# Kernel optimization log

Hardware: AMD Instinct MI355X
Metric: run time of the kernel (lower is better)

The kernel has to match this reference:

```python
import jax, jax.numpy as jnp
import numpy as np

N = 4096        # n_locations
D_MODEL = 512
H, D_K, D_V = 4, 128, 256


def setup_inputs() -> dict:
    key = jax.random.key(0)
    ks = jax.random.split(key, 7)
    s = 0.02
    return {
        "Q": jax.random.normal(ks[0], (N, D_MODEL), dtype=jnp.float32),
        "K": jax.random.normal(ks[1], (N, D_MODEL), dtype=jnp.float32),
        "V": jax.random.normal(ks[2], (N, D_MODEL), dtype=jnp.float32),
        "Wq": jax.random.normal(ks[3], (H, D_MODEL, D_K), dtype=jnp.float32) * s,
        "Wk": jax.random.normal(ks[4], (H, D_MODEL, D_K), dtype=jnp.float32) * s,
        "Wv": jax.random.normal(ks[5], (H, D_MODEL, D_V), dtype=jnp.float32) * s,
        "Wo": jax.random.normal(ks[6], (D_MODEL, H * D_V), dtype=jnp.float32) * s,
    }


def reference(Q, K, V, Wq, Wk, Wv, Wo):
    n = K.shape[0]
    # Batched per-head projections: [h, n, d_k] / [h, n, d_v]
    q = jnp.einsum('nd,hdk->hnk', Q, Wq)
    k = jnp.einsum('nd,hdk->hnk', K, Wk)
    v = jnp.einsum('nd,hdv->hnv', V, Wv)
    # NOTE: original scales by sqrt(n_locations) (K.size(0)), not sqrt(d_k)
    scores = jnp.einsum('hqk,hnk->hqn', q, k) / jnp.sqrt(jnp.asarray(n, q.dtype))
    weights = jax.nn.softmax(scores, axis=-1)          # [h, n, n]
    heads = jnp.einsum('hqn,hnv->hqv', weights, v)      # [h, n, d_v]
    # concat heads along feature dim: [n, h*d_v]
    x = jnp.transpose(heads, (1, 0, 2)).reshape(heads.shape[1], -1)
    return x @ Wo.T                                     # [n, d_model]
```

## Files before the change

### kernel.cpp

```cpp
#include <hip/hip_runtime.h>
#include <hip/hip_bf16.h>
#include <type_traits>

typedef __hip_bfloat16 bf16;
typedef __attribute__((ext_vector_type(8))) short bf16x8;
typedef __attribute__((ext_vector_type(4))) float f32x4;

#define N_LOC 4096

__device__ __forceinline__ bf16 to_bf16(float f) { return __float2bfloat16(f); }

__device__ __forceinline__ void dma16(const bf16* g, bf16* l) {
  __builtin_amdgcn_global_load_lds((const __attribute__((address_space(1))) unsigned int*)g,
                                   (__attribute__((address_space(3))) unsigned int*)l, 16, 0, 0);
}

__global__ __launch_bounds__(256) void prep(const float* __restrict__ Q, const float* __restrict__ K,
                                            const float* __restrict__ V, const float* __restrict__ Wo,
                                            bf16* __restrict__ Qb, bf16* __restrict__ Kb,
                                            bf16* __restrict__ Vb, bf16* __restrict__ Wob,
                                            const float* __restrict__ Wq, const float* __restrict__ Wk,
                                            const float* __restrict__ Wv,
                                            bf16* __restrict__ oq, bf16* __restrict__ ok,
                                            bf16* __restrict__ ov) {
  __shared__ float tile[64][65];
  if (blockIdx.x < 3328) {
    long i = ((long)blockIdx.x * 256 + threadIdx.x) * 8;
    const float* src;
    bf16* dst;
    long off;
    if (i < 2097152)      { src = Q;  dst = Qb;  off = i; }
    else if (i < 4194304) { src = K;  dst = Kb;  off = i - 2097152; }
    else if (i < 6291456) { src = V;  dst = Vb;  off = i - 4194304; }
    else                  { src = Wo; dst = Wob; off = i - 6291456; }
    float4 a = *(const float4*)&src[off];
    float4 b = *(const float4*)&src[off + 4];
    union { bf16 h[8]; bf16x8 v; } u;
    u.h[0] = to_bf16(a.x); u.h[1] = to_bf16(a.y); u.h[2] = to_bf16(a.z); u.h[3] = to_bf16(a.w);
    u.h[4] = to_bf16(b.x); u.h[5] = to_bf16(b.y); u.h[6] = to_bf16(b.z); u.h[7] = to_bf16(b.w);
    *(bf16x8*)&dst[off] = u.v;
  } else {
    int pid = blockIdx.x - 3328;
    int z = pid >> 7;
    int rem = pid & 127;
    int xx = rem & 7, y = rem >> 3;
    const float* W = (z == 0) ? Wq : (z == 1) ? Wk : Wv;
    bf16* out = (z == 0) ? oq : (z == 1) ? ok : ov;
    int DH = (z == 2) ? 256 : 128;
    int nt = DH >> 6;
    if (y >= 4 * nt) return;
    int h = y / nt, tt = y - h * nt;
    int d0 = xx * 64, t0 = tt * 64;
    for (int i = threadIdx.x; i < 4096; i += 256) {
      int r = i >> 6, c = i & 63;
      tile[r][c] = W[((size_t)h * 512 + d0 + r) * DH + t0 + c];
    }
    __syncthreads();
    for (int i = threadIdx.x; i < 4096; i += 256) {
      int t = i >> 6, d = i & 63;
      out[((size_t)(h * DH + t0 + t)) * 512 + d0 + d] = to_bf16(tile[d][t]);
    }
  }
}

template <int BN, int MODE, typename OutT>
__device__ __forceinline__ void gemm_body(const bf16* __restrict__ A, const bf16* __restrict__ Bt,
                                          OutT* __restrict__ C, int N, int K, int m0, int n0,
                                          bf16* sm) {
  constexpr int WN = BN / 2, JN = WN / 16, NB = BN / 32;
  int tid = threadIdx.x, lane = tid & 63, w = tid >> 6;
  int quad = lane >> 4, l16 = lane & 15;
  int wm = (w >> 1) * 64, wn = (w & 1) * WN;
  int srow = lane >> 3;
  int sG = (lane & 7) ^ srow;

  bf16* Asb[2] = { sm, sm + 8192 };
  bf16* Bsb[2] = { sm + 16384, sm + 16384 + BN * 64 };

  const bf16* ga[4];
  const bf16* gb[NB];
#pragma unroll
  for (int j = 0; j < 4; j++) ga[j] = A + (long)(m0 + (4 * j + w) * 8 + srow) * K + sG * 8;
#pragma unroll
  for (int j = 0; j < NB; j++) gb[j] = Bt + (long)(n0 + (4 * j + w) * 8 + srow) * K + sG * 8;

  auto stage = [&](int b) {
#pragma unroll
    for (int j = 0; j < 4; j++) { dma16(ga[j], &Asb[b][(4 * j + w) * 512]); ga[j] += 64; }
#pragma unroll
    for (int j = 0; j < NB; j++) { dma16(gb[j], &Bsb[b][(4 * j + w) * 512]); gb[j] += 64; }
  };

  f32x4 acc[4][JN] = {};
  stage(0);
  asm volatile("" ::: "memory");
  int cur = 0;
  const int NK = K >> 6;
  for (int s = 0; s < NK; ++s) {
    if (s + 1 < NK) {
      stage(cur ^ 1);
      if constexpr (NB == 4) asm volatile("s_waitcnt vmcnt(8)" ::: "memory");
      else                   asm volatile("s_waitcnt vmcnt(6)" ::: "memory");
    } else {
      asm volatile("s_waitcnt vmcnt(0)" ::: "memory");
    }
    __builtin_amdgcn_s_barrier();
    asm volatile("" ::: "memory");
    const bf16* Ac = Asb[cur];
    const bf16* Bc = Bsb[cur];
#pragma unroll
    for (int kk = 0; kk < 2; kk++) {
      bf16x8 af[4], bfr[JN];
#pragma unroll
      for (int i = 0; i < 4; i++) {
        int r = wm + i * 16 + l16;
        af[i] = *(const bf16x8*)&Ac[r * 64 + (((kk * 4 + quad) ^ r) & 7) * 8];
      }
#pragma unroll
      for (int j = 0; j < JN; j++) {
        int r = wn + j * 16 + l16;
        bfr[j] = *(const bf16x8*)&Bc[r * 64 + (((kk * 4 + quad) ^ r) & 7) * 8];
      }
#pragma unroll
      for (int i = 0; i < 4; i++)
#pragma unroll
        for (int j = 0; j < JN; j++)
          acc[i][j] = __builtin_amdgcn_mfma_f32_16x16x32_bf16(af[i], bfr[j], acc[i][j], 0, 0, 0);
    }
    asm volatile("" ::: "memory");
    __builtin_amdgcn_s_barrier();
    asm volatile("" ::: "memory");
    cur ^= 1;
  }

  if constexpr (MODE == 2) {
    bf16* tp = sm;
#pragma unroll
    for (int i = 0; i < 4; i++)
#pragma unroll
      for (int j = 0; j < JN; j++)
#pragma unroll
        for (int r = 0; r < 4; r++)
          tp[(wn + j * 16 + l16) * 136 + wm + i * 16 + quad * 4 + r] = to_bf16(acc[i][j][r]);
    __syncthreads();
#pragma unroll
    for (int it = 0; it < 8; ++it) {
      int idx = it * 256 + tid;
      int rown = idx >> 4, c8 = (idx & 15) * 8;
      *(bf16x8*)&C[(size_t)(n0 + rown) * 4096 + m0 + c8] = *(const bf16x8*)&tp[rown * 136 + c8];
    }
  } else {
#pragma unroll
    for (int i = 0; i < 4; i++)
#pragma unroll
      for (int j = 0; j < JN; j++)
#pragma unroll
        for (int r = 0; r < 4; r++) {
          long row = m0 + wm + i * 16 + quad * 4 + r;
          long col = n0 + wn + j * 16 + l16;
          if constexpr (MODE == 0)
            C[row * N + col] = to_bf16(acc[i][j][r]);
          else
            C[row * N + col] = acc[i][j][r];
        }
  }
}

__global__ __launch_bounds__(256) void proj_gemm(const bf16* __restrict__ QKVb,
                                                 const bf16* __restrict__ Wt,
                                                 bf16* __restrict__ qkout,
                                                 bf16* __restrict__ vTout) {
  __shared__ __align__(16) bf16 sm[4 * 128 * 64];
  int bid = blockIdx.x;
  if (bid < 256) {
    int z = bid >> 7;
    int t = bid & 127;
    int m0 = (t & 31) * 128, n0 = (t >> 5) * 128;
    gemm_body<128, 0, bf16>(QKVb + (size_t)z * 2097152, Wt + (size_t)z * 262144,
                            qkout + (size_t)z * 2097152, 512, 512, m0, n0, sm);
  } else {
    int t = bid - 256;
    int m0 = (t & 31) * 128, n0 = (t >> 5) * 128;
    gemm_body<128, 2, bf16>(QKVb + (size_t)2 * 2097152, Wt + (size_t)2 * 262144,
                            vTout, 1024, 512, m0, n0, sm);
  }
}

__global__ __launch_bounds__(256) void out_gemm(const bf16* __restrict__ xin,
                                                const bf16* __restrict__ Wob,
                                                float* __restrict__ outp) {
  __shared__ __align__(16) bf16 sm[2 * 128 * 64 + 2 * 64 * 64];
  gemm_body<64, 1, float>(xin, Wob, outp, 512, 1024, blockIdx.x * 128, blockIdx.y * 64, sm);
}

__global__ __launch_bounds__(256, 2) void attn(const bf16* __restrict__ qb,
                                               const bf16* __restrict__ kb,
                                               const bf16* __restrict__ vT,
                                               bf16* __restrict__ x) {
  __shared__ __align__(16) bf16 kt[2][64 * 128];
  __shared__ __align__(16) bf16 vt[2][128 * 64];
  __shared__ __align__(16) bf16 pt[4 * 16 * 72];

  const int bid = blockIdx.x;
  const int xcd = bid & 7;
  const int head = xcd & 3;
  const int dvh = xcd >> 2;
  const int q0 = (bid >> 3) * 64;
  const int tid = threadIdx.x;
  const int lane = tid & 63, w = tid >> 6;
  const int quad = lane >> 4, l16 = lane & 15;
  const int qw = q0 + w * 16;
  bf16* ptw = &pt[w * 16 * 72];

  bf16x8 qfB[4];
  {
    const bf16* qrow = &qb[(size_t)(qw + l16) * 512 + head * 128];
#pragma unroll
    for (int kk = 0; kk < 4; kk++) qfB[kk] = *(const bf16x8*)&qrow[kk * 32 + quad * 8];
  }

  f32x4 oacc[8] = {};
  float Lp = 0.0f;
  const float scale = 1.0f / 64.0f;

  const bf16* kpa[4];
  const bf16* vpa[4];
#pragma unroll
  for (int t2 = 0; t2 < 4; t2++) {
    int j = 4 * w + t2;
    {
      int r = 4 * j + (lane >> 4);
      int p = lane & 15;
      int G = (p & 8) | ((p ^ r) & 7);
      kpa[t2] = kb + (size_t)r * 512 + head * 128 + G * 8;
    }
    {
      int r = 8 * j + (lane >> 3);
      int p = lane & 7;
      int G = (p ^ r) & 7;
      vpa[t2] = vT + (size_t)(head * 256 + dvh * 128 + r) * 4096 + G * 8;
    }
  }
  auto STAGE = [&](int b) {
#pragma unroll
    for (int t2 = 0; t2 < 4; t2++) {
      dma16(kpa[t2], &kt[b][(4 * w + t2) * 512]); kpa[t2] += 64 * 512;
      dma16(vpa[t2], &vt[b][(4 * w + t2) * 512]); vpa[t2] += 64;
    }
  };

  STAGE(0);
  asm volatile("" ::: "memory");
  int cur = 0;

  for (int t = 0; t < 64; ++t) {
    asm volatile("s_waitcnt vmcnt(0)" ::: "memory");
    __builtin_amdgcn_s_barrier();
    asm volatile("" ::: "memory");
    if (t < 63) STAGE(cur ^ 1);

    const bf16* ktc = kt[cur];
    f32x4 sacc[4] = {};
#pragma unroll
    for (int kb4 = 0; kb4 < 4; kb4++) {
      int R = kb4 * 16 + l16;
#pragma unroll
      for (int kk = 0; kk < 4; kk++) {
        int G = kk * 4 + quad;
        bf16x8 kf = *(const bf16x8*)&ktc[R * 128 + (((G ^ R) & 7) | (G & 8)) * 8];
        sacc[kb4] = __builtin_amdgcn_mfma_f32_16x16x32_bf16(kf, qfB[kk], sacc[kb4], 0, 0, 0);
      }
    }

#pragma unroll
    for (int kb4 = 0; kb4 < 4; kb4++) {
      float p0 = __expf(sacc[kb4][0] * scale);
      float p1 = __expf(sacc[kb4][1] * scale);
      float p2 = __expf(sacc[kb4][2] * scale);
      float p3 = __expf(sacc[kb4][3] * scale);
      Lp += (p0 + p1) + (p2 + p3);
      union { bf16 h[4]; uint2 u; } pk;
      pk.h[0] = to_bf16(p0); pk.h[1] = to_bf16(p1);
      pk.h[2] = to_bf16(p2); pk.h[3] = to_bf16(p3);
      *(uint2*)&ptw[l16 * 72 + kb4 * 16 + quad * 4] = pk.u;
    }

    const bf16* vtc = vt[cur];
#pragma unroll
    for (int kk = 0; kk < 2; kk++) {
      bf16x8 pf = *(const bf16x8*)&ptw[l16 * 72 + kk * 32 + quad * 8];
#pragma unroll
      for (int c = 0; c < 8; c++) {
        int R = c * 16 + l16;
        int G = kk * 4 + quad;
        bf16x8 vf = *(const bf16x8*)&vtc[R * 64 + ((G ^ R) & 7) * 8];
        oacc[c] = __builtin_amdgcn_mfma_f32_16x16x32_bf16(vf, pf, oacc[c], 0, 0, 0);
      }
    }
    cur ^= 1;
  }

  float Lf = Lp;
  Lf += __shfl_xor(Lf, 16);
  Lf += __shfl_xor(Lf, 32);
  float inv = 1.0f / Lf;

#pragma unroll
  for (int c = 0; c < 8; c++) {
    union { bf16 h[4]; uint2 u; } ok;
    ok.h[0] = to_bf16(oacc[c][0] * inv);
    ok.h[1] = to_bf16(oacc[c][1] * inv);
    ok.h[2] = to_bf16(oacc[c][2] * inv);
    ok.h[3] = to_bf16(oacc[c][3] * inv);
    *(uint2*)&x[(size_t)(qw + l16) * 1024 + head * 256 + dvh * 128 + c * 16 + quad * 4] = ok.u;
  }
}

extern "C" void kernel_launch(void* const* d_in, const int* in_sizes, int n_in,
                              void* d_out, int out_size, void* d_ws, size_t ws_size,
                              hipStream_t stream) {
  const float* Q  = (const float*)d_in[0];
  const float* Km = (const float*)d_in[1];
  const float* V  = (const float*)d_in[2];
  const float* Wq = (const float*)d_in[3];
  const float* Wk = (const float*)d_in[4];
  const float* Wv = (const float*)d_in[5];
  const float* Wo = (const float*)d_in[6];
  float* out = (float*)d_out;

  bf16* ws  = (bf16*)d_ws;
  bf16* Qb  = ws;
  bf16* Kb  = Qb + 2097152;
  bf16* Vb  = Kb + 2097152;
  bf16* Wqt = Vb + 2097152;
  bf16* Wkt = Wqt + 262144;
  bf16* Wvt = Wkt + 262144;
  bf16* Wob = Wvt + 524288;
  bf16* qb  = Wob + 524288;
  bf16* kb  = qb + 2097152;
  bf16* vT  = kb + 2097152;
  bf16* x   = vT + 4194304;

  prep<<<3712, 256, 0, stream>>>(Q, Km, V, Wo, Qb, Kb, Vb, Wob, Wq, Wk, Wv, Wqt, Wkt, Wvt);

  proj_gemm<<<512, 256, 0, stream>>>(Qb, Wqt, qb, vT);

  attn<<<512, 256, 0, stream>>>(qb, kb, vT, x);

  out_gemm<<<dim3(32, 8), 256, 0, stream>>>(x, Wob, out);
}
```

Baseline: 224.7 us.

## Switch attention to 32x32x16 MFMA with 128-query tiles and register P transpose

The attention kernel moves from 16x16x32 to 32x32x16 bf16 MFMA. Each wave now owns 32 queries and each block 128, so the grid halves to 256 blocks. The P tile no longer round-trips through LDS: it is rearranged in registers with v_permlane32_swap, and the output is stored with a different lane mapping. This is meant to reuse each staged K/V tile across twice as many queries and cut LDS traffic, at the cost of higher register pressure and fewer blocks to fill the CUs.

```diff
diff --git a/kernel.cpp b/kernel.cpp
--- a/kernel.cpp
+++ b/kernel.cpp
@@ -5,6 +5,7 @@
 typedef __hip_bfloat16 bf16;
 typedef __attribute__((ext_vector_type(8))) short bf16x8;
 typedef __attribute__((ext_vector_type(4))) float f32x4;
+typedef __attribute__((ext_vector_type(16))) float f32x16;
 
 #define N_LOC 4096
 
@@ -199,27 +200,25 @@
                                                bf16* __restrict__ x) {
   __shared__ __align__(16) bf16 kt[2][64 * 128];
   __shared__ __align__(16) bf16 vt[2][128 * 64];
-  __shared__ __align__(16) bf16 pt[4 * 16 * 72];
 
   const int bid = blockIdx.x;
   const int xcd = bid & 7;
   const int head = xcd & 3;
   const int dvh = xcd >> 2;
-  const int q0 = (bid >> 3) * 64;
+  const int q0 = (bid >> 3) * 128;
   const int tid = threadIdx.x;
   const int lane = tid & 63, w = tid >> 6;
-  const int quad = lane >> 4, l16 = lane & 15;
-  const int qw = q0 + w * 16;
-  bf16* ptw = &pt[w * 16 * 72];
-
-  bf16x8 qfB[4];
+  const int l32 = lane & 31, hi = lane >> 5;
+  const int qw = q0 + w * 32;
+
+  bf16x8 qfB[8];
   {
-    const bf16* qrow = &qb[(size_t)(qw + l16) * 512 + head * 128];
-#pragma unroll
-    for (int kk = 0; kk < 4; kk++) qfB[kk] = *(const bf16x8*)&qrow[kk * 32 + quad * 8];
-  }
-
-  f32x4 oacc[8] = {};
+    const bf16* qrow = &qb[(size_t)(qw + l32) * 512 + head * 128];
+#pragma unroll
+    for (int c = 0; c < 8; c++) qfB[c] = *(const bf16x8*)&qrow[c * 16 + hi * 8];
+  }
+
+  f32x16 oacc[4] = {};
   float Lp = 0.0f;
   const float scale = 1.0f / 64.0f;
 
@@ -260,60 +259,64 @@
     if (t < 63) STAGE(cur ^ 1);
 
     const bf16* ktc = kt[cur];
-    f32x4 sacc[4] = {};
-#pragma unroll
-    for (int kb4 = 0; kb4 < 4; kb4++) {
-      int R = kb4 * 16 + l16;
-#pragma unroll
-      for (int kk = 0; kk < 4; kk++) {
-        int G = kk * 4 + quad;
-        bf16x8 kf = *(const bf16x8*)&ktc[R * 128 + (((G ^ R) & 7) | (G & 8)) * 8];
-        sacc[kb4] = __builtin_amdgcn_mfma_f32_16x16x32_bf16(kf, qfB[kk], sacc[kb4], 0, 0, 0);
+    f32x16 s0 = {}, s1 = {};
+#pragma unroll
+    for (int c = 0; c < 8; c++) {
+      int G = c * 2 + hi;
+      int p8 = (((G ^ l32) & 7) | (G & 8)) * 8;
+      bf16x8 kf0 = *(const bf16x8*)&ktc[l32 * 128 + p8];
+      bf16x8 kf1 = *(const bf16x8*)&ktc[(32 + l32) * 128 + p8];
+      s0 = __builtin_amdgcn_mfma_f32_32x32x16_bf16(kf0, qfB[c], s0, 0, 0, 0);
+      s1 = __builtin_amdgcn_mfma_f32_32x32x16_bf16(kf1, qfB[c], s1, 0, 0, 0);
+    }
+
+    unsigned pk[16];
+#pragma unroll
+    for (int i = 0; i < 8; i++) {
+      float p0 = __expf(s0[2 * i] * scale), p1 = __expf(s0[2 * i + 1] * scale);
+      float p2 = __expf(s1[2 * i] * scale), p3 = __expf(s1[2 * i + 1] * scale);
+      Lp += (p0 + p1) + (p2 + p3);
+      union { bf16 h[2]; unsigned u; } a0, a1;
+      a0.h[0] = to_bf16(p0); a0.h[1] = to_bf16(p1);
+      a1.h[0] = to_bf16(p2); a1.h[1] = to_bf16(p3);
+      pk[i] = a0.u;
+      pk[8 + i] = a1.u;
+    }
+
+    const bf16* vtc = vt[cur];
+#pragma unroll
+    for (int c = 0; c < 4; c++) {
+      unsigned w0 = pk[c * 4 + 0], w1 = pk[c * 4 + 1];
+      unsigned w2 = pk[c * 4 + 2], w3 = pk[c * 4 + 3];
+      asm("v_permlane32_swap_b32 %0, %1" : "+v"(w0), "+v"(w2));
+      asm("v_permlane32_swap_b32 %0, %1" : "+v"(w1), "+v"(w3));
+      union { unsigned u[4]; bf16x8 v; } pb;
+      pb.u[0] = w0; pb.u[1] = w1; pb.u[2] = w2; pb.u[3] = w3;
+      int G = c * 2 + hi;
+#pragma unroll
+      for (int d = 0; d < 4; d++) {
+        int R = d * 32 + l32;
+        bf16x8 vf = *(const bf16x8*)&vtc[R * 64 + ((G ^ R) & 7) * 8];
+        oacc[d] = __builtin_amdgcn_mfma_f32_32x32x16_bf16(vf, pb.v, oacc[d], 0, 0, 0);
       }
     }
-
-#pragma unroll
-    for (int kb4 = 0; kb4 < 4; kb4++) {
-      float p0 = __expf(sacc[kb4][0] * scale);
-      float p1 = __expf(sacc[kb4][1] * scale);
-      float p2 = __expf(sacc[kb4][2] * scale);
-      float p3 = __expf(sacc[kb4][3] * scale);
-      Lp += (p0 + p1) + (p2 + p3);
-      union { bf16 h[4]; uint2 u; } pk;
-      pk.h[0] = to_bf16(p0); pk.h[1] = to_bf16(p1);
-      pk.h[2] = to_bf16(p2); pk.h[3] = to_bf16(p3);
-      *(uint2*)&ptw[l16 * 72 + kb4 * 16 + quad * 4] = pk.u;
-    }
-
-    const bf16* vtc = vt[cur];
-#pragma unroll
-    for (int kk = 0; kk < 2; kk++) {
-      bf16x8 pf = *(const bf16x8*)&ptw[l16 * 72 + kk * 32 + quad * 8];
-#pragma unroll
-      for (int c = 0; c < 8; c++) {
-        int R = c * 16 + l16;
-        int G = kk * 4 + quad;
-        bf16x8 vf = *(const bf16x8*)&vtc[R * 64 + ((G ^ R) & 7) * 8];
-        oacc[c] = __builtin_amdgcn_mfma_f32_16x16x32_bf16(vf, pf, oacc[c], 0, 0, 0);
-      }
-    }
     cur ^= 1;
   }
 
-  float Lf = Lp;
-  Lf += __shfl_xor(Lf, 16);
-  Lf += __shfl_xor(Lf, 32);
+  float Lf = Lp + __shfl_xor(Lp, 32);
   float inv = 1.0f / Lf;
 
-#pragma unroll
-  for (int c = 0; c < 8; c++) {
-    union { bf16 h[4]; uint2 u; } ok;
-    ok.h[0] = to_bf16(oacc[c][0] * inv);
-    ok.h[1] = to_bf16(oacc[c][1] * inv);
-    ok.h[2] = to_bf16(oacc[c][2] * inv);
-    ok.h[3] = to_bf16(oacc[c][3] * inv);
-    *(uint2*)&x[(size_t)(qw + l16) * 1024 + head * 256 + dvh * 128 + c * 16 + quad * 4] = ok.u;
-  }
+  bf16* xrow = &x[(size_t)(qw + l32) * 1024 + head * 256 + dvh * 128];
+#pragma unroll
+  for (int d = 0; d < 4; d++)
+#pragma unroll
+    for (int i = 0; i < 8; i++) {
+      int dvp = d * 32 + 2 * (i & 1) + 8 * (i >> 1) + 4 * hi;
+      union { bf16 h[2]; unsigned u; } o2;
+      o2.h[0] = to_bf16(oacc[d][2 * i] * inv);
+      o2.h[1] = to_bf16(oacc[d][2 * i + 1] * inv);
+      *(unsigned*)&xrow[dvp] = o2.u;
+    }
 }
 
 extern "C" void kernel_launch(void* const* d_in, const int* in_sizes, int n_in,
@@ -345,7 +348,7 @@
 
   proj_gemm<<<512, 256, 0, stream>>>(Qb, Wqt, qb, vT);
 
-  attn<<<512, 256, 0, stream>>>(qb, kb, vT, x);
+  attn<<<256, 256, 0, stream>>>(qb, kb, vT, x);
 
   out_gemm<<<dim3(32, 8), 256, 0, stream>>>(x, Wob, out);
 }
```

Result: slower. 238.0 us (+5.9%).
